# Kernel tuning notes

Hardware: AMD Instinct MI355X
Metric: run time of the kernel (lower is better)

The kernel has to match this reference:

```python
import jax, jax.numpy as jnp
import numpy as np

B, N, H, W = 2, 1024, 128, 128
SH_K = 27  # (sh_degree+1)^2 * 3 for sh_degree=2
L_L1, L_SSIM, L_DEPTH, L_OPAC = 0.8, 0.2, 0.5, 0.01
C0 = 0.28209479177387814


def _quat_to_rot(q):
    # q: [..., 4] (w,x,y,z) -> [..., 3, 3]
    w, x, y, z = q[..., 0], q[..., 1], q[..., 2], q[..., 3]
    R = jnp.stack([1 - 2 * (y * y + z * z), 2 * (x * y - w * z), 2 * (x * z + w * y),
                   2 * (x * y + w * z), 1 - 2 * (x * x + z * z), 2 * (y * z - w * x),
                   2 * (x * z - w * y), 2 * (y * z + w * x), 1 - 2 * (x * x + y * y)], axis=-1)
    return R.reshape(q.shape[:-1] + (3, 3))


def _ssim_window(size=7, sigma=1.5):
    coords = np.arange(size, dtype=np.float32) - size // 2
    g = np.exp(-coords ** 2 / (2 * sigma ** 2))
    g = g / g.sum()
    w2 = np.outer(g, g).astype(np.float32)
    return jnp.asarray(np.broadcast_to(w2[None, None], (3, 1, size, size)))  # OIHW, groups=3


def _dwconv(img, w):
    return jax.lax.conv_general_dilated(img, w, (1, 1), 'SAME',
                                        dimension_numbers=('NCHW', 'OIHW', 'NCHW'),
                                        feature_group_count=3)


def _ssim(img1, img2):
    C1, C2 = 0.01 ** 2, 0.03 ** 2
    w = _ssim_window()
    mu1, mu2 = _dwconv(img1, w), _dwconv(img2, w)
    s1 = _dwconv(img1 * img1, w) - mu1 ** 2
    s2 = _dwconv(img2 * img2, w) - mu2 ** 2
    s12 = _dwconv(img1 * img2, w) - mu1 * mu2
    return jnp.mean((2 * mu1 * mu2 + C1) * (2 * s12 + C2) /
                    ((mu1 ** 2 + mu2 ** 2 + C1) * (s1 + s2 + C2)))


def _render(gaussians, intrinsics):
    means = gaussians[:, :, :3]
    scales = gaussians[:, :, 3:6]
    rots = gaussians[:, :, 6:10]
    opac = gaussians[:, :, 10]        # [B,N]
    sh = gaussians[:, :, 11:]
    fx = intrinsics[:, 0, 0][:, None]
    fy = intrinsics[:, 1, 1][:, None]
    cx = intrinsics[:, 0, 2][:, None]
    cy = intrinsics[:, 1, 2][:, None]
    z = jnp.maximum(means[:, :, 2], 1e-4)
    px = fx * means[:, :, 0] / z + cx
    py = fy * means[:, :, 1] / z + cy
    # ---- 2D covariance (EWA) ----
    R = _quat_to_rot(rots)                               # [B,N,3,3]
    RS = R * scales[:, :, None, :]                        # R @ diag(s)
    cov3d = RS @ jnp.swapaxes(RS, -1, -2)
    zc = jnp.maximum(means[:, :, 2], 1e-6)
    zsq = zc * zc
    J = jnp.zeros(means.shape[:2] + (2, 3), means.dtype)
    J = J.at[:, :, 0, 0].set(fx / zc)
    J = J.at[:, :, 0, 2].set(-fx * means[:, :, 0] / zsq)
    J = J.at[:, :, 1, 1].set(fy / zc)
    J = J.at[:, :, 1, 2].set(-fy * means[:, :, 1] / zsq)
    cov2d = J @ cov3d @ jnp.swapaxes(J, -1, -2) + 0.3 * jnp.eye(2, dtype=means.dtype)
    det = jnp.maximum(cov2d[:, :, 0, 0] * cov2d[:, :, 1, 1] -
                      cov2d[:, :, 0, 1] * cov2d[:, :, 1, 0], 1e-8)
    inv00 = cov2d[:, :, 1, 1] / det
    inv11 = cov2d[:, :, 0, 0] / det
    inv01 = -cov2d[:, :, 0, 1] / det
    colors = jnp.clip(sh[:, :, :3] * C0 + 0.5, 0.0, 1.0)  # [B,N,3]
    # ---- dense per-pixel splatting ----
    gy = jnp.arange(H, dtype=means.dtype)
    gx = jnp.arange(W, dtype=means.dtype)
    dx = gx[None, None, None, :] - px[:, :, None, None]   # [B,N,1,W] -> bcast [B,N,H,W]
    dy = gy[None, None, :, None] - py[:, :, None, None]
    power = -0.5 * (inv00[:, :, None, None] * dx * dx +
                    2.0 * inv01[:, :, None, None] * dx * dy +
                    inv11[:, :, None, None] * dy * dy)
    alpha = jnp.exp(jnp.clip(power, -10.0, 0.0)) * opac[:, :, None, None]
    alpha = jnp.minimum(alpha, 0.99)
    # ---- depth sort + front-to-back compositing ----
    order = jnp.argsort(z, axis=1)
    alpha_s = jnp.take_along_axis(alpha, order[:, :, None, None], axis=1)
    colors_s = jnp.take_along_axis(colors, order[:, :, None], axis=1)
    depth_s = jnp.take_along_axis(z, order, axis=1)
    cp = jnp.cumprod(1.0 - alpha_s, axis=1)
    Tr = jnp.concatenate([jnp.ones_like(alpha_s[:, :1]), cp[:, :-1]], axis=1)
    weights = Tr * alpha_s                               # [B,N,H,W]
    rgb = jnp.clip(jnp.einsum('bnhw,bnc->bchw', weights, colors_s), 0.0, 1.0)
    depth = jnp.sum(weights * depth_s[:, :, None, None], axis=1, keepdims=True)
    return rgb, depth


def setup_inputs() -> dict:
    key = jax.random.key(0)
    k = jax.random.split(key, 8)
    xy = jax.random.normal(k[0], (B, N, 2)) * 1.0
    zc = jax.random.uniform(k[1], (B, N, 1), minval=0.5, maxval=4.0)
    scales = jax.random.uniform(k[2], (B, N, 3), minval=0.01, maxval=0.1)
    q = jax.random.normal(k[3], (B, N, 4))
    q = q / jnp.linalg.norm(q, axis=-1, keepdims=True)
    opac = jax.nn.sigmoid(jax.random.normal(k[4], (B, N, 1)))
    sh = jax.random.normal(k[5], (B, N, SH_K)) * 0.3
    gaussians = jnp.concatenate([xy, zc, scales, q, opac, sh], axis=-1)  # [B,N,38]
    intr = jnp.tile(jnp.array([[120.0, 0.0, 64.0], [0.0, 120.0, 64.0], [0.0, 0.0, 1.0]],
                              dtype=jnp.float32)[None], (B, 1, 1))
    target_rgb = jax.random.uniform(k[6], (B, 3, H, W))
    target_depth = jax.random.uniform(k[7], (B, 1, H, W), minval=0.5, maxval=4.0)
    return {'gaussians': gaussians, 'intrinsics': intr,
            'target_rgb': target_rgb, 'target_depth': target_depth}


def reference(gaussians, intrinsics, target_rgb, target_depth):
    rgb, depth = _render(gaussians, intrinsics)
    l1_rgb = jnp.mean(jnp.abs(rgb - target_rgb))
    ssim_val = _ssim(rgb, target_rgb)
    l1_depth = jnp.mean(jnp.abs(depth - target_depth))
    o = jnp.clip(gaussians[:, :, 10:11], 1e-6, 1.0 - 1e-6)
    opacity_reg = jnp.mean(-(o * jnp.log(o) + (1.0 - o) * jnp.log(1.0 - o)))
    loss = (L_L1 * l1_rgb + L_SSIM * (1.0 - ssim_val) +
            L_DEPTH * l1_depth + L_OPAC * opacity_reg)
    return loss
```

## Files before the change

kernel.cpp:

```cpp
#include <hip/hip_runtime.h>

#define NB 2
#define NG 1024
#define HEIGHT 128
#define WIDTH 128
#define HW (HEIGHT * WIDTH)
#define E10 4.5399931e-05f

#define REC_U 0
#define REC_S 32768
#define Z_U   65536
#define PFX   67584
#define TCNT  83984
#define TLIST 84496
#define RGBOF 346640
#define P_ENT 444944
#define P_L1D 444952
#define P_SSS 445464
#define P_SSL 445848

__device__ inline float blk_reduce(float v, float* sh) {
    for (int off = 32; off > 0; off >>= 1) v += __shfl_down(v, off, 64);
    int lane = threadIdx.x & 63;
    int w = threadIdx.x >> 6;
    __syncthreads();
    if (lane == 0) sh[w] = v;
    __syncthreads();
    float s = 0.f;
    if (threadIdx.x == 0) {
        int nw = (blockDim.x + 63) >> 6;
        for (int i = 0; i < nw; i++) s += sh[i];
    }
    return s;
}

__global__ __launch_bounds__(256) void k_pre(const float* __restrict__ g,
                                             const float* __restrict__ intr,
                                             float* __restrict__ ws) {
    __shared__ float sh[8];
    int idx = blockIdx.x * 256 + threadIdx.x;
    int b = idx >> 10;
    const float* row = g + (size_t)idx * 38;
    float mx = row[0], my = row[1], mz = row[2];
    float sx = row[3], sy = row[4], sz = row[5];
    float qw = row[6], qx = row[7], qy = row[8], qz = row[9];
    float op = row[10];
    float sh0 = row[11], sh1 = row[12], sh2 = row[13];
    float fx = intr[b * 9 + 0], fy = intr[b * 9 + 4];
    float cx = intr[b * 9 + 2], cy = intr[b * 9 + 5];

    float z = fmaxf(mz, 1e-4f);
    float px = fx * mx / z + cx;
    float py = fy * my / z + cy;

    float r00 = 1.f - 2.f * (qy * qy + qz * qz), r01 = 2.f * (qx * qy - qw * qz), r02 = 2.f * (qx * qz + qw * qy);
    float r10 = 2.f * (qx * qy + qw * qz), r11 = 1.f - 2.f * (qx * qx + qz * qz), r12 = 2.f * (qy * qz - qw * qx);
    float r20 = 2.f * (qx * qz - qw * qy), r21 = 2.f * (qy * qz + qw * qx), r22 = 1.f - 2.f * (qx * qx + qy * qy);
    float a00 = r00 * sx, a01 = r01 * sy, a02 = r02 * sz;
    float a10 = r10 * sx, a11 = r11 * sy, a12 = r12 * sz;
    float a20 = r20 * sx, a21 = r21 * sy, a22 = r22 * sz;
    float m00 = a00 * a00 + a01 * a01 + a02 * a02;
    float m01 = a00 * a10 + a01 * a11 + a02 * a12;
    float m02 = a00 * a20 + a01 * a21 + a02 * a22;
    float m11 = a10 * a10 + a11 * a11 + a12 * a12;
    float m12 = a10 * a20 + a11 * a21 + a12 * a22;
    float m22 = a20 * a20 + a21 * a21 + a22 * a22;

    float zc = fmaxf(mz, 1e-6f);
    float aJ = fx / zc, bJ = -fx * mx / (zc * zc);
    float cJ = fy / zc, dJ = -fy * my / (zc * zc);
    float c00 = aJ * aJ * m00 + 2.f * aJ * bJ * m02 + bJ * bJ * m22 + 0.3f;
    float c01 = cJ * (aJ * m01 + bJ * m12) + dJ * (aJ * m02 + bJ * m22);
    float c11 = cJ * cJ * m11 + 2.f * cJ * dJ * m12 + dJ * dJ * m22 + 0.3f;
    float det = fmaxf(c00 * c11 - c01 * c01, 1e-8f);
    float i00 = c11 / det;
    float i11 = c00 / det;
    float i01 = -c01 / det;

    const float C0c = 0.28209479177387814f;
    float col0 = fminf(fmaxf(sh0 * C0c + 0.5f, 0.f), 1.f);
    float col1 = fminf(fmaxf(sh1 * C0c + 0.5f, 0.f), 1.f);
    float col2 = fminf(fmaxf(sh2 * C0c + 0.5f, 0.f), 1.f);

    float hx = sqrtf(20.f * c00);
    float hy = sqrtf(20.f * c11);

    float* rec = ws + REC_U + (size_t)idx * 16;
    rec[0] = px; rec[1] = py; rec[2] = hx; rec[3] = hy;
    rec[4] = i00; rec[5] = i01; rec[6] = i11; rec[7] = op;
    rec[8] = col0; rec[9] = col1; rec[10] = col2; rec[11] = z;
    rec[12] = E10 * op; rec[13] = 0.f; rec[14] = 0.f; rec[15] = 0.f;
    ws[Z_U + idx] = z;

    float o = fminf(fmaxf(op, 1e-6f), 1.f - 1e-6f);
    float ent = -(o * logf(o) + (1.f - o) * logf(1.f - o));
    float s = blk_reduce(ent, sh);
    if (threadIdx.x == 0) ws[P_ENT + blockIdx.x] = s;
}

__global__ __launch_bounds__(256) void k_rank(float* __restrict__ ws) {
    __shared__ float zs[NG];
    __shared__ int sp[256];
    int bid = blockIdx.x;
    int b = bid >> 4;
    int grp = bid & 15;
    int tid = threadIdx.x;
    const float* zb = ws + Z_U + (b << 10);
    ((float4*)zs)[tid] = ((const float4*)zb)[tid];
    __syncthreads();
    int il = (grp << 6) + (tid & 63);
    int jq = tid >> 6;
    float zi = zs[il];
    int rank = 0;
    int j0 = jq << 8;
#pragma unroll 4
    for (int j = j0; j < j0 + 256; j += 4) {
        float4 zq = *(const float4*)(zs + j);
        rank += (zq.x < zi) || (zq.x == zi && (j + 0) < il);
        rank += (zq.y < zi) || (zq.y == zi && (j + 1) < il);
        rank += (zq.z < zi) || (zq.z == zi && (j + 2) < il);
        rank += (zq.w < zi) || (zq.w == zi && (j + 3) < il);
    }
    sp[tid] = rank;
    __syncthreads();
    if (tid < 64) {
        int r = sp[tid] + sp[tid + 64] + sp[tid + 128] + sp[tid + 192];
        int gi = (b << 10) + il;
        const float4* src = (const float4*)(ws + REC_U + (size_t)gi * 16);
        float4 r0 = src[0], r1 = src[1], r2 = src[2], r3 = src[3];
        float4* dst = (float4*)(ws + REC_S + (size_t)((b << 10) + r) * 16);
        dst[0] = r0; dst[1] = r1; dst[2] = r2; dst[3] = r3;
    }
}

__global__ __launch_bounds__(1024) void k_scan(float* __restrict__ ws) {
    __shared__ float st[NG], sur[NG], sug[NG], sub_[NG], sud[NG];
    int b = blockIdx.x;
    int k = threadIdx.x;
    const float* r = ws + REC_S + (size_t)((b << 10) + k) * 16;
    float4 f1 = ((const float4*)r)[1];
    float4 f2 = ((const float4*)r)[2];
    float a10 = E10 * f1.w;
    st[k] = 1.f - a10;
    sur[k] = a10 * f2.x; sug[k] = a10 * f2.y; sub_[k] = a10 * f2.z; sud[k] = a10 * f2.w;
    __syncthreads();
    for (int off = 1; off < NG; off <<= 1) {
        float tl = 1.f, url = 0.f, ugl = 0.f, ubl = 0.f, udl = 0.f;
        if (k >= off) {
            tl = st[k - off]; url = sur[k - off]; ugl = sug[k - off];
            ubl = sub_[k - off]; udl = sud[k - off];
        }
        __syncthreads();
        if (k >= off) {
            sur[k] = url + tl * sur[k];
            sug[k] = ugl + tl * sug[k];
            sub_[k] = ubl + tl * sub_[k];
            sud[k] = udl + tl * sud[k];
            st[k] = tl * st[k];
        }
        __syncthreads();
    }
    float* P = ws + PFX + (size_t)b * 8200;
    ((float4*)(P + (size_t)(k + 1) * 8))[0] = make_float4(st[k], sur[k], sug[k], sub_[k]);
    P[(size_t)(k + 1) * 8 + 4] = sud[k];
    if (k == 0) {
        ((float4*)P)[0] = make_float4(1.f, 0.f, 0.f, 0.f);
        P[4] = 0.f;
    }
}

__global__ __launch_bounds__(256) void k_bin(float* __restrict__ ws) {
    __shared__ int sc[256];
    int blk = blockIdx.x;
    int b = blk >> 8;
    int t = blk & 255;
    float x0f = (float)((t & 15) * 8), x1f = x0f + 7.f;
    float y0f = (float)((t >> 4) * 8), y1f = y0f + 7.f;
    int tid = threadIdx.x;
    int r0 = tid * 4;
    int pred = 0;
#pragma unroll
    for (int j = 0; j < 4; j++) {
        float4 bb = ((const float4*)(ws + REC_S + (size_t)((b << 10) + r0 + j) * 16))[0];
        bool ov = (bb.x + bb.z >= x0f) && (bb.x - bb.z <= x1f) &&
                  (bb.y + bb.w >= y0f) && (bb.y - bb.w <= y1f);
        pred |= (int)ov << j;
    }
    int cnt = __popc(pred);
    sc[tid] = cnt;
    __syncthreads();
    for (int off = 1; off < 256; off <<= 1) {
        int v = 0;
        if (tid >= off) v = sc[tid - off];
        __syncthreads();
        sc[tid] += v;
        __syncthreads();
    }
    unsigned short* list = (unsigned short*)(ws + TLIST) + (size_t)blk * 1024;
    int pos = sc[tid] - cnt;
#pragma unroll
    for (int j = 0; j < 4; j++)
        if (pred & (1 << j)) list[pos++] = (unsigned short)(r0 + j);
    if (tid == 255) ((int*)(ws + TCNT))[blk] = sc[255];
}

__global__ __launch_bounds__(1024, 8) void k_render(const float* __restrict__ tgt_d,
                                                    float* __restrict__ ws) {
    __shared__ float comb[5][1024];
    int tid = threadIdx.x;
    int lane = tid & 63;
    int wv = tid >> 6;
    int blk = blockIdx.x;
    int b = blk >> 8;
    int t = blk & 255;
    int x0 = (t & 15) * 8, y0 = (t >> 4) * 8;
    int x = x0 + (lane & 7), y = y0 + (lane >> 3);
    float xf = (float)x, yf = (float)y;

    int cnt = ((const int*)(ws + TCNT))[blk];
    const unsigned short* list = (const unsigned short*)(ws + TLIST) + (size_t)blk * 1024;
    const float* P = ws + PFX + (size_t)b * 8200;
    const float* recs = ws + REC_S + (size_t)(b << 10) * 16;

    int m = (cnt + 15) >> 4;
    int p0 = wv * m; if (p0 > cnt) p0 = cnt;
    int p1 = p0 + m; if (p1 > cnt) p1 = cnt;
    int s0 = (p0 == 0) ? 0 : (int)list[p0 - 1] + 1;

    float4 Pa = *(const float4*)(P + (size_t)s0 * 8);
    float Pud = P[(size_t)s0 * 8 + 4];
    float inv0 = 1.f / Pa.x;
    float Pur = Pa.y, Pug = Pa.z, Pub = Pa.w;

    float tau = 1.f, cr = 0.f, cg = 0.f, cb = 0.f, cd = 0.f;
    for (int p = p0; p < p1; p++) {
        int r = (int)list[p];
        float4 Qa = *(const float4*)(P + (size_t)r * 8);
        float Qud = P[(size_t)r * 8 + 4];
        const float* rec = recs + (size_t)r * 16;
        float4 g0 = ((const float4*)rec)[0];
        float4 g1 = ((const float4*)rec)[1];
        float4 g2 = ((const float4*)rec)[2];
        float kap = tau * inv0;
        cr += kap * (Qa.y - Pur);
        cg += kap * (Qa.z - Pug);
        cb += kap * (Qa.w - Pub);
        cd += kap * (Qud - Pud);
        float dx = xf - g0.x, dy = yf - g0.y;
        float q = g1.x * dx * dx + 2.f * g1.y * dx * dy + g1.z * dy * dy;
        float pw = fminf(fmaxf(-0.5f * q, -10.f), 0.f);
        float a = fminf(__expf(pw) * g1.w, 0.99f);
        float w = kap * Qa.x * a;
        cr += w * g2.x; cg += w * g2.y; cb += w * g2.z; cd += w * g2.w;
        float a10 = E10 * g1.w;
        tau *= (1.f - a) * (1.f + a10 * (1.f + a10));
        float s = Qa.x * a10;
        Pur = Qa.y + s * g2.x;
        Pug = Qa.z + s * g2.y;
        Pub = Qa.w + s * g2.z;
        Pud = Qud + s * g2.w;
    }
    int e0 = (wv == 15) ? NG : ((p1 == 0) ? 0 : (int)list[p1 - 1] + 1);
    float4 Ea = *(const float4*)(P + (size_t)e0 * 8);
    float Eud = P[(size_t)e0 * 8 + 4];
    float kapf = tau * inv0;
    cr += kapf * (Ea.y - Pur);
    cg += kapf * (Ea.z - Pug);
    cb += kapf * (Ea.w - Pub);
    cd += kapf * (Eud - Pud);
    float T = tau * Ea.x * inv0;

    comb[0][tid] = T;
    comb[1][tid] = cr;
    comb[2][tid] = cg;
    comb[3][tid] = cb;
    comb[4][tid] = cd;
    __syncthreads();

    if (tid < 64) {
        float T0 = comb[0][tid], r0 = comb[1][tid], g0 = comb[2][tid];
        float b0 = comb[3][tid], d0 = comb[4][tid];
#pragma unroll
        for (int sgi = 1; sgi < 16; sgi++) {
            int j = sgi * 64 + tid;
            r0 += T0 * comb[1][j];
            g0 += T0 * comb[2][j];
            b0 += T0 * comb[3][j];
            d0 += T0 * comb[4][j];
            T0 *= comb[0][j];
        }
        r0 = fminf(fmaxf(r0, 0.f), 1.f);
        g0 = fminf(fmaxf(g0, 0.f), 1.f);
        b0 = fminf(fmaxf(b0, 0.f), 1.f);
        float* rgb = ws + RGBOF;
        rgb[((b * 3 + 0) * HEIGHT + y) * WIDTH + x] = r0;
        rgb[((b * 3 + 1) * HEIGHT + y) * WIDTH + x] = g0;
        rgb[((b * 3 + 2) * HEIGHT + y) * WIDTH + x] = b0;
        float l1d = fabsf(d0 - tgt_d[(b * HEIGHT + y) * WIDTH + x]);
        for (int off = 32; off > 0; off >>= 1) l1d += __shfl_down(l1d, off, 64);
        if (tid == 0) ws[P_L1D + blk] = l1d;
    }
}

__global__ __launch_bounds__(256) void k_ssim(const float* __restrict__ tgt_rgb,
                                              float* __restrict__ ws) {
    __shared__ float sh[8];
    int idx = blockIdx.x * 256 + threadIdx.x;
    const float* img1 = ws + RGBOF;
    int bc = idx >> 14;
    int pix = idx & (HW - 1);
    int y = pix >> 7, x = pix & 127;

    float gg[7];
    float gs = 0.f;
#pragma unroll
    for (int i = 0; i < 7; i++) {
        float c = (float)(i - 3);
        gg[i] = __expf(-c * c / 4.5f);
        gs += gg[i];
    }
#pragma unroll
    for (int i = 0; i < 7; i++) gg[i] /= gs;

    float mu1 = 0.f, mu2 = 0.f, s11 = 0.f, s22 = 0.f, s12 = 0.f;
    int plane = bc * HW;
#pragma unroll
    for (int dy = -3; dy <= 3; dy++) {
        int yy = y + dy;
#pragma unroll
        for (int dx = -3; dx <= 3; dx++) {
            int xx = x + dx;
            float w = gg[dy + 3] * gg[dx + 3];
            float i1 = 0.f, i2 = 0.f;
            if (yy >= 0 && yy < HEIGHT && xx >= 0 && xx < WIDTH) {
                int o = plane + yy * WIDTH + xx;
                i1 = img1[o];
                i2 = tgt_rgb[o];
            }
            mu1 += w * i1;
            mu2 += w * i2;
            s11 += w * i1 * i1;
            s22 += w * i2 * i2;
            s12 += w * i1 * i2;
        }
    }
    float v1 = s11 - mu1 * mu1;
    float v2 = s22 - mu2 * mu2;
    float cv = s12 - mu1 * mu2;
    const float C1 = 1e-4f, C2 = 9e-4f;
    float ssim = ((2.f * mu1 * mu2 + C1) * (2.f * cv + C2)) /
                 ((mu1 * mu1 + mu2 * mu2 + C1) * (v1 + v2 + C2));
    float l1 = fabsf(img1[idx] - tgt_rgb[idx]);

    float s_ssim = blk_reduce(ssim, sh);
    float s_l1 = blk_reduce(l1, sh);
    if (threadIdx.x == 0) {
        ws[P_SSS + blockIdx.x] = s_ssim;
        ws[P_SSL + blockIdx.x] = s_l1;
    }
}

__global__ __launch_bounds__(256) void k_final(const float* __restrict__ ws_c,
                                               float* __restrict__ out) {
    __shared__ float sh[8];
    float e = 0.f, d = 0.f, ss = 0.f, sl = 0.f;
    for (int i = threadIdx.x; i < 512; i += 256) d += ws_c[P_L1D + i];
    for (int i = threadIdx.x; i < 384; i += 256) { ss += ws_c[P_SSS + i]; sl += ws_c[P_SSL + i]; }
    if (threadIdx.x < 8) e = ws_c[P_ENT + threadIdx.x];
    float rd_ = blk_reduce(d, sh);
    float rss = blk_reduce(ss, sh);
    float rsl = blk_reduce(sl, sh);
    float re = blk_reduce(e, sh);
    if (threadIdx.x == 0) {
        float l1r = rsl / (float)(NB * 3 * HW);
        float ssim = rss / (float)(NB * 3 * HW);
        float l1d = rd_ / (float)(NB * HW);
        float opa = re / (float)(NB * NG);
        out[0] = 0.8f * l1r + 0.2f * (1.f - ssim) + 0.5f * l1d + 0.01f * opa;
    }
}

extern "C" void kernel_launch(void* const* d_in, const int* in_sizes, int n_in,
                              void* d_out, int out_size, void* d_ws, size_t ws_size,
                              hipStream_t stream) {
    const float* g = (const float*)d_in[0];
    const float* intr = (const float*)d_in[1];
    const float* trgb = (const float*)d_in[2];
    const float* tdep = (const float*)d_in[3];
    float* ws = (float*)d_ws;
    float* out = (float*)d_out;

    hipLaunchKernelGGL(k_pre, dim3(8), dim3(256), 0, stream, g, intr, ws);
    hipLaunchKernelGGL(k_rank, dim3(32), dim3(256), 0, stream, ws);
    hipLaunchKernelGGL(k_scan, dim3(NB), dim3(1024), 0, stream, ws);
    hipLaunchKernelGGL(k_bin, dim3(NB * 256), dim3(256), 0, stream, ws);
    hipLaunchKernelGGL(k_render, dim3(NB * 256), dim3(1024), 0, stream, tdep, ws);
    hipLaunchKernelGGL(k_ssim, dim3((NB * 3 * HW) / 256), dim3(256), 0, stream, trgb, ws);
    hipLaunchKernelGGL(k_final, dim3(1), dim3(256), 0, stream, ws, out);
}
```

Before: 97.65 us.

## Fuse preprocessing into ranking and binning/scan into render, merge final reduction

New measurement: 95.94 us. No clear change (-1.8%).

```diff
diff --git a/kernel.cpp b/kernel.cpp
--- a/kernel.cpp
+++ b/kernel.cpp
@@ -7,17 +7,13 @@
 #define HW (HEIGHT * WIDTH)
 #define E10 4.5399931e-05f
 
-#define REC_U 0
-#define REC_S 32768
-#define Z_U   65536
-#define PFX   67584
-#define TCNT  83984
-#define TLIST 84496
-#define RGBOF 346640
-#define P_ENT 444944
-#define P_L1D 444952
-#define P_SSS 445464
-#define P_SSL 445848
+#define REC_S 0
+#define P_ENT 32768
+#define P_L1D 32800
+#define P_SSS 33312
+#define P_SSL 33696
+#define CNT_I 34080
+#define RGBOF 34084
 
 __device__ inline float blk_reduce(float v, float* sh) {
     for (int off = 32; off > 0; off >>= 1) v += __shfl_down(v, off, 64);
@@ -34,245 +30,231 @@
     return s;
 }
 
-__global__ __launch_bounds__(256) void k_pre(const float* __restrict__ g,
-                                             const float* __restrict__ intr,
-                                             float* __restrict__ ws) {
-    __shared__ float sh[8];
-    int idx = blockIdx.x * 256 + threadIdx.x;
-    int b = idx >> 10;
-    const float* row = g + (size_t)idx * 38;
-    float mx = row[0], my = row[1], mz = row[2];
-    float sx = row[3], sy = row[4], sz = row[5];
-    float qw = row[6], qx = row[7], qy = row[8], qz = row[9];
-    float op = row[10];
-    float sh0 = row[11], sh1 = row[12], sh2 = row[13];
-    float fx = intr[b * 9 + 0], fy = intr[b * 9 + 4];
-    float cx = intr[b * 9 + 2], cy = intr[b * 9 + 5];
-
-    float z = fmaxf(mz, 1e-4f);
-    float px = fx * mx / z + cx;
-    float py = fy * my / z + cy;
-
-    float r00 = 1.f - 2.f * (qy * qy + qz * qz), r01 = 2.f * (qx * qy - qw * qz), r02 = 2.f * (qx * qz + qw * qy);
-    float r10 = 2.f * (qx * qy + qw * qz), r11 = 1.f - 2.f * (qx * qx + qz * qz), r12 = 2.f * (qy * qz - qw * qx);
-    float r20 = 2.f * (qx * qz - qw * qy), r21 = 2.f * (qy * qz + qw * qx), r22 = 1.f - 2.f * (qx * qx + qy * qy);
-    float a00 = r00 * sx, a01 = r01 * sy, a02 = r02 * sz;
-    float a10 = r10 * sx, a11 = r11 * sy, a12 = r12 * sz;
-    float a20 = r20 * sx, a21 = r21 * sy, a22 = r22 * sz;
-    float m00 = a00 * a00 + a01 * a01 + a02 * a02;
-    float m01 = a00 * a10 + a01 * a11 + a02 * a12;
-    float m02 = a00 * a20 + a01 * a21 + a02 * a22;
-    float m11 = a10 * a10 + a11 * a11 + a12 * a12;
-    float m12 = a10 * a20 + a11 * a21 + a12 * a22;
-    float m22 = a20 * a20 + a21 * a21 + a22 * a22;
-
-    float zc = fmaxf(mz, 1e-6f);
-    float aJ = fx / zc, bJ = -fx * mx / (zc * zc);
-    float cJ = fy / zc, dJ = -fy * my / (zc * zc);
-    float c00 = aJ * aJ * m00 + 2.f * aJ * bJ * m02 + bJ * bJ * m22 + 0.3f;
-    float c01 = cJ * (aJ * m01 + bJ * m12) + dJ * (aJ * m02 + bJ * m22);
-    float c11 = cJ * cJ * m11 + 2.f * cJ * dJ * m12 + dJ * dJ * m22 + 0.3f;
-    float det = fmaxf(c00 * c11 - c01 * c01, 1e-8f);
-    float i00 = c11 / det;
-    float i11 = c00 / det;
-    float i01 = -c01 / det;
-
-    const float C0c = 0.28209479177387814f;
-    float col0 = fminf(fmaxf(sh0 * C0c + 0.5f, 0.f), 1.f);
-    float col1 = fminf(fmaxf(sh1 * C0c + 0.5f, 0.f), 1.f);
-    float col2 = fminf(fmaxf(sh2 * C0c + 0.5f, 0.f), 1.f);
-
-    float hx = sqrtf(20.f * c00);
-    float hy = sqrtf(20.f * c11);
-
-    float* rec = ws + REC_U + (size_t)idx * 16;
-    rec[0] = px; rec[1] = py; rec[2] = hx; rec[3] = hy;
-    rec[4] = i00; rec[5] = i01; rec[6] = i11; rec[7] = op;
-    rec[8] = col0; rec[9] = col1; rec[10] = col2; rec[11] = z;
-    rec[12] = E10 * op; rec[13] = 0.f; rec[14] = 0.f; rec[15] = 0.f;
-    ws[Z_U + idx] = z;
-
-    float o = fminf(fmaxf(op, 1e-6f), 1.f - 1e-6f);
-    float ent = -(o * logf(o) + (1.f - o) * logf(1.f - o));
-    float s = blk_reduce(ent, sh);
-    if (threadIdx.x == 0) ws[P_ENT + blockIdx.x] = s;
-}
-
-__global__ __launch_bounds__(256) void k_rank(float* __restrict__ ws) {
-    __shared__ float zs[NG];
+__global__ __launch_bounds__(256) void k_prerank(const float* __restrict__ g,
+                                                 const float* __restrict__ intr,
+                                                 float* __restrict__ ws) {
+    __shared__ __align__(16) unsigned long long zkey[NG];
     __shared__ int sp[256];
     int bid = blockIdx.x;
     int b = bid >> 4;
     int grp = bid & 15;
     int tid = threadIdx.x;
-    const float* zb = ws + Z_U + (b << 10);
-    ((float4*)zs)[tid] = ((const float4*)zb)[tid];
-    __syncthreads();
+
+#pragma unroll
+    for (int q = 0; q < 4; q++) {
+        int j = tid + q * 256;
+        float z = fmaxf(g[(size_t)((b << 10) + j) * 38 + 2], 1e-4f);
+        zkey[j] = ((unsigned long long)__float_as_uint(z) << 10) | (unsigned)j;
+    }
+    __syncthreads();
+
     int il = (grp << 6) + (tid & 63);
     int jq = tid >> 6;
-    float zi = zs[il];
+    unsigned long long ki = zkey[il];
     int rank = 0;
     int j0 = jq << 8;
 #pragma unroll 4
-    for (int j = j0; j < j0 + 256; j += 4) {
-        float4 zq = *(const float4*)(zs + j);
-        rank += (zq.x < zi) || (zq.x == zi && (j + 0) < il);
-        rank += (zq.y < zi) || (zq.y == zi && (j + 1) < il);
-        rank += (zq.z < zi) || (zq.z == zi && (j + 2) < il);
-        rank += (zq.w < zi) || (zq.w == zi && (j + 3) < il);
+    for (int j = j0; j < j0 + 256; j += 2) {
+        ulonglong2 kk = *(const ulonglong2*)(zkey + j);
+        rank += (kk.x < ki);
+        rank += (kk.y < ki);
     }
     sp[tid] = rank;
     __syncthreads();
+
     if (tid < 64) {
         int r = sp[tid] + sp[tid + 64] + sp[tid + 128] + sp[tid + 192];
-        int gi = (b << 10) + il;
-        const float4* src = (const float4*)(ws + REC_U + (size_t)gi * 16);
-        float4 r0 = src[0], r1 = src[1], r2 = src[2], r3 = src[3];
-        float4* dst = (float4*)(ws + REC_S + (size_t)((b << 10) + r) * 16);
-        dst[0] = r0; dst[1] = r1; dst[2] = r2; dst[3] = r3;
-    }
-}
-
-__global__ __launch_bounds__(1024) void k_scan(float* __restrict__ ws) {
-    __shared__ float st[NG], sur[NG], sug[NG], sub_[NG], sud[NG];
-    int b = blockIdx.x;
-    int k = threadIdx.x;
-    const float* r = ws + REC_S + (size_t)((b << 10) + k) * 16;
-    float4 f1 = ((const float4*)r)[1];
-    float4 f2 = ((const float4*)r)[2];
-    float a10 = E10 * f1.w;
-    st[k] = 1.f - a10;
-    sur[k] = a10 * f2.x; sug[k] = a10 * f2.y; sub_[k] = a10 * f2.z; sud[k] = a10 * f2.w;
-    __syncthreads();
-    for (int off = 1; off < NG; off <<= 1) {
-        float tl = 1.f, url = 0.f, ugl = 0.f, ubl = 0.f, udl = 0.f;
-        if (k >= off) {
-            tl = st[k - off]; url = sur[k - off]; ugl = sug[k - off];
-            ubl = sub_[k - off]; udl = sud[k - off];
-        }
-        __syncthreads();
-        if (k >= off) {
-            sur[k] = url + tl * sur[k];
-            sug[k] = ugl + tl * sug[k];
-            sub_[k] = ubl + tl * sub_[k];
-            sud[k] = udl + tl * sud[k];
-            st[k] = tl * st[k];
-        }
-        __syncthreads();
-    }
-    float* P = ws + PFX + (size_t)b * 8200;
-    ((float4*)(P + (size_t)(k + 1) * 8))[0] = make_float4(st[k], sur[k], sug[k], sub_[k]);
-    P[(size_t)(k + 1) * 8 + 4] = sud[k];
-    if (k == 0) {
-        ((float4*)P)[0] = make_float4(1.f, 0.f, 0.f, 0.f);
-        P[4] = 0.f;
-    }
-}
-
-__global__ __launch_bounds__(256) void k_bin(float* __restrict__ ws) {
-    __shared__ int sc[256];
-    int blk = blockIdx.x;
-    int b = blk >> 8;
-    int t = blk & 255;
-    float x0f = (float)((t & 15) * 8), x1f = x0f + 7.f;
-    float y0f = (float)((t >> 4) * 8), y1f = y0f + 7.f;
-    int tid = threadIdx.x;
-    int r0 = tid * 4;
-    int pred = 0;
-#pragma unroll
-    for (int j = 0; j < 4; j++) {
-        float4 bb = ((const float4*)(ws + REC_S + (size_t)((b << 10) + r0 + j) * 16))[0];
-        bool ov = (bb.x + bb.z >= x0f) && (bb.x - bb.z <= x1f) &&
-                  (bb.y + bb.w >= y0f) && (bb.y - bb.w <= y1f);
-        pred |= (int)ov << j;
-    }
-    int cnt = __popc(pred);
-    sc[tid] = cnt;
-    __syncthreads();
-    for (int off = 1; off < 256; off <<= 1) {
-        int v = 0;
-        if (tid >= off) v = sc[tid - off];
-        __syncthreads();
-        sc[tid] += v;
-        __syncthreads();
-    }
-    unsigned short* list = (unsigned short*)(ws + TLIST) + (size_t)blk * 1024;
-    int pos = sc[tid] - cnt;
-#pragma unroll
-    for (int j = 0; j < 4; j++)
-        if (pred & (1 << j)) list[pos++] = (unsigned short)(r0 + j);
-    if (tid == 255) ((int*)(ws + TCNT))[blk] = sc[255];
+        int idx = (b << 10) + il;
+        const float* row = g + (size_t)idx * 38;
+        float mx = row[0], my = row[1], mz = row[2];
+        float sx = row[3], sy = row[4], sz = row[5];
+        float qw = row[6], qx = row[7], qy = row[8], qz = row[9];
+        float op = row[10];
+        float sh0 = row[11], sh1 = row[12], sh2 = row[13];
+        float fx = intr[b * 9 + 0], fy = intr[b * 9 + 4];
+        float cx = intr[b * 9 + 2], cy = intr[b * 9 + 5];
+
+        float z = fmaxf(mz, 1e-4f);
+        float px = fx * mx / z + cx;
+        float py = fy * my / z + cy;
+
+        float r00 = 1.f - 2.f * (qy * qy + qz * qz), r01 = 2.f * (qx * qy - qw * qz), r02 = 2.f * (qx * qz + qw * qy);
+        float r10 = 2.f * (qx * qy + qw * qz), r11 = 1.f - 2.f * (qx * qx + qz * qz), r12 = 2.f * (qy * qz - qw * qx);
+        float r20 = 2.f * (qx * qz - qw * qy), r21 = 2.f * (qy * qz + qw * qx), r22 = 1.f - 2.f * (qx * qx + qy * qy);
+        float a00 = r00 * sx, a01 = r01 * sy, a02 = r02 * sz;
+        float a10 = r10 * sx, a11 = r11 * sy, a12 = r12 * sz;
+        float a20 = r20 * sx, a21 = r21 * sy, a22 = r22 * sz;
+        float m00 = a00 * a00 + a01 * a01 + a02 * a02;
+        float m01 = a00 * a10 + a01 * a11 + a02 * a12;
+        float m02 = a00 * a20 + a01 * a21 + a02 * a22;
+        float m11 = a10 * a10 + a11 * a11 + a12 * a12;
+        float m12 = a10 * a20 + a11 * a21 + a12 * a22;
+        float m22 = a20 * a20 + a21 * a21 + a22 * a22;
+
+        float zc = fmaxf(mz, 1e-6f);
+        float aJ = fx / zc, bJ = -fx * mx / (zc * zc);
+        float cJ = fy / zc, dJ = -fy * my / (zc * zc);
+        float c00 = aJ * aJ * m00 + 2.f * aJ * bJ * m02 + bJ * bJ * m22 + 0.3f;
+        float c01 = cJ * (aJ * m01 + bJ * m12) + dJ * (aJ * m02 + bJ * m22);
+        float c11 = cJ * cJ * m11 + 2.f * cJ * dJ * m12 + dJ * dJ * m22 + 0.3f;
+        float det = fmaxf(c00 * c11 - c01 * c01, 1e-8f);
+        float i00 = c11 / det;
+        float i11 = c00 / det;
+        float i01 = -c01 / det;
+
+        const float C0c = 0.28209479177387814f;
+        float col0 = fminf(fmaxf(sh0 * C0c + 0.5f, 0.f), 1.f);
+        float col1 = fminf(fmaxf(sh1 * C0c + 0.5f, 0.f), 1.f);
+        float col2 = fminf(fmaxf(sh2 * C0c + 0.5f, 0.f), 1.f);
+
+        float hx = sqrtf(20.f * c00);
+        float hy = sqrtf(20.f * c11);
+
+        float* rec = ws + REC_S + (size_t)((b << 10) + r) * 16;
+        ((float4*)rec)[0] = make_float4(px, py, hx, hy);
+        ((float4*)rec)[1] = make_float4(i00, i01, i11, op);
+        ((float4*)rec)[2] = make_float4(col0, col1, col2, z);
+
+        float o = fminf(fmaxf(op, 1e-6f), 1.f - 1e-6f);
+        float ent = -(o * logf(o) + (1.f - o) * logf(1.f - o));
+        for (int off = 32; off > 0; off >>= 1) ent += __shfl_down(ent, off, 64);
+        if (tid == 0) ws[P_ENT + bid] = ent;
+    }
+    if (bid == 0 && tid == 0) ((int*)ws)[CNT_I] = 0;
 }
 
 __global__ __launch_bounds__(1024, 8) void k_render(const float* __restrict__ tgt_d,
                                                     float* __restrict__ ws) {
+    __shared__ float4 sPa[NG + 1];
+    __shared__ float sPud[NG + 1];
+    __shared__ unsigned short slist[NG];
+    __shared__ int swcnt[16];
+    __shared__ float sagg[16 * 5];
     __shared__ float comb[5][1024];
+
     int tid = threadIdx.x;
     int lane = tid & 63;
     int wv = tid >> 6;
     int blk = blockIdx.x;
     int b = blk >> 8;
-    int t = blk & 255;
-    int x0 = (t & 15) * 8, y0 = (t >> 4) * 8;
+    int tt = blk & 255;
+    int x0 = (tt & 15) * 8, y0 = (tt >> 4) * 8;
     int x = x0 + (lane & 7), y = y0 + (lane >> 3);
     float xf = (float)x, yf = (float)y;
-
-    int cnt = ((const int*)(ws + TCNT))[blk];
-    const unsigned short* list = (const unsigned short*)(ws + TLIST) + (size_t)blk * 1024;
-    const float* P = ws + PFX + (size_t)b * 8200;
+    float x0f = (float)x0, x1f = x0f + 7.f;
+    float y0f = (float)y0, y1f = y0f + 7.f;
+
     const float* recs = ws + REC_S + (size_t)(b << 10) * 16;
+
+    const float* rec = recs + (size_t)tid * 16;
+    float4 q0 = ((const float4*)rec)[0];
+    float4 q1 = ((const float4*)rec)[1];
+    float4 q2 = ((const float4*)rec)[2];
+
+    bool ov = (q0.x + q0.z >= x0f) && (q0.x - q0.z <= x1f) &&
+              (q0.y + q0.w >= y0f) && (q0.y - q0.w <= y1f);
+    unsigned long long mask = __ballot(ov);
+    int loff = __popcll(mask & ((1ull << lane) - 1ull));
+    if (lane == 0) swcnt[wv] = (int)__popcll(mask);
+
+    float a10 = E10 * q1.w;
+    float t = 1.f - a10;
+    float ur = a10 * q2.x, ug = a10 * q2.y, ub = a10 * q2.z, ud = a10 * q2.w;
+#pragma unroll
+    for (int off = 1; off < 64; off <<= 1) {
+        float pt = __shfl_up(t, off, 64);
+        float pr = __shfl_up(ur, off, 64);
+        float pg = __shfl_up(ug, off, 64);
+        float pb = __shfl_up(ub, off, 64);
+        float pd = __shfl_up(ud, off, 64);
+        if (lane >= off) {
+            ur = pr + pt * ur; ug = pg + pt * ug;
+            ub = pb + pt * ub; ud = pd + pt * ud;
+            t = pt * t;
+        }
+    }
+    if (lane == 63) {
+        sagg[wv * 5 + 0] = t;  sagg[wv * 5 + 1] = ur; sagg[wv * 5 + 2] = ug;
+        sagg[wv * 5 + 3] = ub; sagg[wv * 5 + 4] = ud;
+    }
+    __syncthreads();
+
+    int woff = 0, cnt = 0;
+#pragma unroll
+    for (int i = 0; i < 16; i++) {
+        int ci = swcnt[i];
+        woff += (i < wv) ? ci : 0;
+        cnt += ci;
+    }
+    if (ov) slist[woff + loff] = (unsigned short)tid;
+
+    float Pt = 1.f, Pur = 0.f, Pug = 0.f, Pub = 0.f, Pud0 = 0.f;
+    for (int i = 0; i < wv; i++) {
+        float at = sagg[i * 5], ar = sagg[i * 5 + 1], ag = sagg[i * 5 + 2];
+        float ab = sagg[i * 5 + 3], ad = sagg[i * 5 + 4];
+        Pur = Pur + Pt * ar; Pug = Pug + Pt * ag;
+        Pub = Pub + Pt * ab; Pud0 = Pud0 + Pt * ad;
+        Pt = Pt * at;
+    }
+    sPa[tid + 1] = make_float4(Pt * t, Pur + Pt * ur, Pug + Pt * ug, Pub + Pt * ub);
+    sPud[tid + 1] = Pud0 + Pt * ud;
+    if (tid == 0) {
+        sPa[0] = make_float4(1.f, 0.f, 0.f, 0.f);
+        sPud[0] = 0.f;
+    }
+    __syncthreads();
 
     int m = (cnt + 15) >> 4;
     int p0 = wv * m; if (p0 > cnt) p0 = cnt;
     int p1 = p0 + m; if (p1 > cnt) p1 = cnt;
-    int s0 = (p0 == 0) ? 0 : (int)list[p0 - 1] + 1;
-
-    float4 Pa = *(const float4*)(P + (size_t)s0 * 8);
-    float Pud = P[(size_t)s0 * 8 + 4];
+    int s0 = (p0 == 0) ? 0 : (int)slist[p0 - 1] + 1;
+
+    float4 Pa = sPa[s0];
+    float Pud = sPud[s0];
     float inv0 = 1.f / Pa.x;
-    float Pur = Pa.y, Pug = Pa.z, Pub = Pa.w;
-
-    float tau = 1.f, cr = 0.f, cg = 0.f, cb = 0.f, cd = 0.f;
+    float Pur2 = Pa.y, Pug2 = Pa.z, Pub2 = Pa.w;
+
+    float tau = 1.f, cr = 0.f, cgn = 0.f, cb = 0.f, cd = 0.f;
     for (int p = p0; p < p1; p++) {
-        int r = (int)list[p];
-        float4 Qa = *(const float4*)(P + (size_t)r * 8);
-        float Qud = P[(size_t)r * 8 + 4];
-        const float* rec = recs + (size_t)r * 16;
-        float4 g0 = ((const float4*)rec)[0];
-        float4 g1 = ((const float4*)rec)[1];
-        float4 g2 = ((const float4*)rec)[2];
+        int r = (int)slist[p];
+        float4 Qa = sPa[r];
+        float Qud = sPud[r];
+        const float* rp = recs + (size_t)r * 16;
+        float4 g0 = ((const float4*)rp)[0];
+        float4 g1 = ((const float4*)rp)[1];
+        float4 g2 = ((const float4*)rp)[2];
         float kap = tau * inv0;
-        cr += kap * (Qa.y - Pur);
-        cg += kap * (Qa.z - Pug);
-        cb += kap * (Qa.w - Pub);
+        cr += kap * (Qa.y - Pur2);
+        cgn += kap * (Qa.z - Pug2);
+        cb += kap * (Qa.w - Pub2);
         cd += kap * (Qud - Pud);
         float dx = xf - g0.x, dy = yf - g0.y;
         float q = g1.x * dx * dx + 2.f * g1.y * dx * dy + g1.z * dy * dy;
         float pw = fminf(fmaxf(-0.5f * q, -10.f), 0.f);
         float a = fminf(__expf(pw) * g1.w, 0.99f);
         float w = kap * Qa.x * a;
-        cr += w * g2.x; cg += w * g2.y; cb += w * g2.z; cd += w * g2.w;
-        float a10 = E10 * g1.w;
-        tau *= (1.f - a) * (1.f + a10 * (1.f + a10));
-        float s = Qa.x * a10;
-        Pur = Qa.y + s * g2.x;
-        Pug = Qa.z + s * g2.y;
-        Pub = Qa.w + s * g2.z;
+        cr += w * g2.x; cgn += w * g2.y; cb += w * g2.z; cd += w * g2.w;
+        float a10i = E10 * g1.w;
+        tau *= (1.f - a) * (1.f + a10i * (1.f + a10i));
+        float s = Qa.x * a10i;
+        Pur2 = Qa.y + s * g2.x;
+        Pug2 = Qa.z + s * g2.y;
+        Pub2 = Qa.w + s * g2.z;
         Pud = Qud + s * g2.w;
     }
-    int e0 = (wv == 15) ? NG : ((p1 == 0) ? 0 : (int)list[p1 - 1] + 1);
-    float4 Ea = *(const float4*)(P + (size_t)e0 * 8);
-    float Eud = P[(size_t)e0 * 8 + 4];
+    int e0 = (wv == 15) ? NG : ((p1 == 0) ? 0 : (int)slist[p1 - 1] + 1);
+    float4 Ea = sPa[e0];
+    float Eud = sPud[e0];
     float kapf = tau * inv0;
-    cr += kapf * (Ea.y - Pur);
-    cg += kapf * (Ea.z - Pug);
-    cb += kapf * (Ea.w - Pub);
+    cr += kapf * (Ea.y - Pur2);
+    cgn += kapf * (Ea.z - Pug2);
+    cb += kapf * (Ea.w - Pub2);
     cd += kapf * (Eud - Pud);
     float T = tau * Ea.x * inv0;
 
     comb[0][tid] = T;
     comb[1][tid] = cr;
-    comb[2][tid] = cg;
+    comb[2][tid] = cgn;
     comb[3][tid] = cb;
     comb[4][tid] = cd;
     __syncthreads();
@@ -302,10 +284,13 @@
     }
 }
 
-__global__ __launch_bounds__(256) void k_ssim(const float* __restrict__ tgt_rgb,
-                                              float* __restrict__ ws) {
+__global__ __launch_bounds__(256) void k_ssim_final(const float* __restrict__ tgt_rgb,
+                                                    float* __restrict__ ws,
+                                                    float* __restrict__ out) {
     __shared__ float sh[8];
-    int idx = blockIdx.x * 256 + threadIdx.x;
+    __shared__ int sflag;
+    int bid = blockIdx.x;
+    int idx = bid * 256 + threadIdx.x;
     const float* img1 = ws + RGBOF;
     int bc = idx >> 14;
     int pix = idx & (HW - 1);
@@ -354,29 +339,32 @@
 
     float s_ssim = blk_reduce(ssim, sh);
     float s_l1 = blk_reduce(l1, sh);
+
     if (threadIdx.x == 0) {
-        ws[P_SSS + blockIdx.x] = s_ssim;
-        ws[P_SSL + blockIdx.x] = s_l1;
-    }
-}
-
-__global__ __launch_bounds__(256) void k_final(const float* __restrict__ ws_c,
-                                               float* __restrict__ out) {
-    __shared__ float sh[8];
-    float e = 0.f, d = 0.f, ss = 0.f, sl = 0.f;
-    for (int i = threadIdx.x; i < 512; i += 256) d += ws_c[P_L1D + i];
-    for (int i = threadIdx.x; i < 384; i += 256) { ss += ws_c[P_SSS + i]; sl += ws_c[P_SSL + i]; }
-    if (threadIdx.x < 8) e = ws_c[P_ENT + threadIdx.x];
-    float rd_ = blk_reduce(d, sh);
-    float rss = blk_reduce(ss, sh);
-    float rsl = blk_reduce(sl, sh);
-    float re = blk_reduce(e, sh);
-    if (threadIdx.x == 0) {
-        float l1r = rsl / (float)(NB * 3 * HW);
-        float ssim = rss / (float)(NB * 3 * HW);
-        float l1d = rd_ / (float)(NB * HW);
-        float opa = re / (float)(NB * NG);
-        out[0] = 0.8f * l1r + 0.2f * (1.f - ssim) + 0.5f * l1d + 0.01f * opa;
+        ws[P_SSS + bid] = s_ssim;
+        ws[P_SSL + bid] = s_l1;
+        __threadfence();
+        int old = atomicAdd((int*)ws + CNT_I, 1);
+        sflag = (old == 383) ? 1 : 0;
+    }
+    __syncthreads();
+    if (sflag) {
+        __threadfence();
+        float d = 0.f, ss = 0.f, sl = 0.f, e = 0.f;
+        for (int i = threadIdx.x; i < 512; i += 256) d += ws[P_L1D + i];
+        for (int i = threadIdx.x; i < 384; i += 256) { ss += ws[P_SSS + i]; sl += ws[P_SSL + i]; }
+        if (threadIdx.x < 32) e = ws[P_ENT + threadIdx.x];
+        float rd_ = blk_reduce(d, sh);
+        float rss = blk_reduce(ss, sh);
+        float rsl = blk_reduce(sl, sh);
+        float re = blk_reduce(e, sh);
+        if (threadIdx.x == 0) {
+            float l1r = rsl / (float)(NB * 3 * HW);
+            float ssimv = rss / (float)(NB * 3 * HW);
+            float l1d = rd_ / (float)(NB * HW);
+            float opa = re / (float)(NB * NG);
+            out[0] = 0.8f * l1r + 0.2f * (1.f - ssimv) + 0.5f * l1d + 0.01f * opa;
+        }
     }
 }
 
@@ -390,11 +378,7 @@
     float* ws = (float*)d_ws;
     float* out = (float*)d_out;
 
-    hipLaunchKernelGGL(k_pre, dim3(8), dim3(256), 0, stream, g, intr, ws);
-    hipLaunchKernelGGL(k_rank, dim3(32), dim3(256), 0, stream, ws);
-    hipLaunchKernelGGL(k_scan, dim3(NB), dim3(1024), 0, stream, ws);
-    hipLaunchKernelGGL(k_bin, dim3(NB * 256), dim3(256), 0, stream, ws);
+    hipLaunchKernelGGL(k_prerank, dim3(32), dim3(256), 0, stream, g, intr, ws);
     hipLaunchKernelGGL(k_render, dim3(NB * 256), dim3(1024), 0, stream, tdep, ws);
-    hipLaunchKernelGGL(k_ssim, dim3((NB * 3 * HW) / 256), dim3(256), 0, stream, trgb, ws);
-    hipLaunchKernelGGL(k_final, dim3(1), dim3(256), 0, stream, ws, out);
-}
+    hipLaunchKernelGGL(k_ssim_final, dim3((NB * 3 * HW) / 256), dim3(256), 0, stream, trgb, ws, out);
+}
```
